# Kernel tuning notes

Measured on AMD Instinct MI355X. Metric: run time of the kernel, lower is better.

## Reference

```python
import jax, jax.numpy as jnp
import numpy as np


def _rotated_kernels(kernel, n_or):
    """Nearest-neighbour rotated copies of the kernel.

    kernel: [C, kOr, kH, kW] -> returns [n_or, C, kOr, kH, kW] where slice t is the
    kernel sampled at R_{2*pi*t/n_or}(y', x') about the kernel center; rotated
    coordinates that fall outside the kernel grid contribute zero.
    """
    C, kOr, kH, kW = kernel.shape
    cy = (kH - 1) / 2.0
    cx = (kW - 1) / 2.0
    ang = 2.0 * jnp.pi * jnp.arange(n_or, dtype=jnp.float32) / n_or
    ca = jnp.cos(ang)[:, None, None]  # [n_or,1,1]
    sa = jnp.sin(ang)[:, None, None]
    yy = jnp.arange(kH, dtype=jnp.float32)[:, None] - cy  # [kH,1]
    xx = jnp.arange(kW, dtype=jnp.float32)[None, :] - cx  # [1,kW]
    # rotate grid points by angle theta
    ys = sa * xx + ca * yy  # [n_or,kH,kW]
    xs = ca * xx - sa * yy
    iy = jnp.round(ys + cy).astype(jnp.int32)
    ix = jnp.round(xs + cx).astype(jnp.int32)
    mask = ((iy >= 0) & (iy < kH) & (ix >= 0) & (ix < kW)).astype(kernel.dtype)
    iyc = jnp.clip(iy, 0, kH - 1)
    ixc = jnp.clip(ix, 0, kW - 1)
    rot = kernel[:, :, iyc, ixc]            # [C,kOr,n_or,kH,kW] (gather)
    rot = rot * mask[None, None]            # zero out-of-grid samples
    return jnp.transpose(rot, (2, 0, 1, 3, 4))  # [n_or,C,kOr,kH,kW]


def setup_inputs() -> dict:
    key = jax.random.key(0)
    k1, k2 = jax.random.split(key)
    B, C, Or, H, W = 8, 32, 8, 128, 128
    kOr, kH, kW = 8, 5, 5
    x = jax.random.normal(k1, (B, C, Or, H, W), dtype=jnp.float32)
    # module parameter: uniform(-1, 1) per reset_parameters()
    kernel = jax.random.uniform(k2, (C, kOr, kH, kW), minval=-1.0, maxval=1.0,
                                dtype=jnp.float32)
    return {"x": x, "kernel": kernel}


def reference(x, kernel):
    """SE(2) linear (depthwise) group convolution.

    out[b,c,t,y,x] = sum_{t',y',x'} x[b,c,(t+t')%Or, y+y', x+x']
                     * kernel[c, t', NN(R_{2pi t/Or}(y', x'))]
    with centered, zero-padded spatial offsets ('SAME').
    """
    B, C, Or, H, W = x.shape
    _, kOr, kH, kW = kernel.shape
    rotk = _rotated_kernels(kernel, Or)  # [Or,C,kOr,kH,kW]
    dn = ('NCHW', 'OIHW', 'NCHW')
    out = jnp.zeros((B, C * Or, H, W), dtype=x.dtype)
    for tp in range(kOr):  # small fixed orientation-offset loop
        xs = jnp.roll(x, -tp, axis=2).reshape(B, C * Or, H, W)  # circular wrap in Or
        k = jnp.transpose(rotk[:, :, tp], (1, 0, 2, 3)).reshape(C * Or, 1, kH, kW)
        out = out + jax.lax.conv_general_dilated(
            xs, k, window_strides=(1, 1), padding='SAME',
            feature_group_count=C * Or, dimension_numbers=dn)
    return out.reshape(B, C, Or, H, W)
```

## Files before the change

kernel.cpp:

```cpp
#include <hip/hip_runtime.h>


typedef short bf16x8 __attribute__((ext_vector_type(8)));
typedef float f32x4 __attribute__((ext_vector_type(4)));

__device__ inline unsigned short f2bf(float f) {
    unsigned int u = __float_as_uint(f);
    u += 0x7fffu + ((u >> 16) & 1u);
    return (unsigned short)(u >> 16);
}
__device__ inline unsigned pk2(float a, float b) {
    return (unsigned)f2bf(a) | ((unsigned)f2bf(b) << 16);
}

__device__ __constant__ float CA8[8] = {1.0f, 0.70710678f, 0.0f, -0.70710678f,
                                        -1.0f, -0.70710678f, 0.0f, 0.70710678f};
__device__ __constant__ float SA8[8] = {0.0f, 0.70710678f, 1.0f, 0.70710678f,
                                        0.0f, -0.70710678f, -1.0f, -0.70710678f};

__global__ __launch_bounds__(256, 5)
void se2_mfma(const float* __restrict__ x, const float* __restrict__ kern,
              float* __restrict__ out) {
    __shared__ __align__(16) unsigned short ldsx[36 * 36 * 8];
    __shared__ __align__(16) unsigned short ldsw[8 * 28 * 8];

    const int bid = (blockIdx.x & 7) * 512 + (blockIdx.x >> 3);
    const int tx = bid & 3, ty = (bid >> 2) & 3;
    const int bc = bid >> 4;
    const int c  = bc & 31;
    const int X0 = tx * 32, Y0 = ty * 32;
    const int tid = threadIdx.x;

    for (int e = tid; e < 1792; e += 256) {
        int t   = e / 224;
        int rem = e - t * 224;
        int tap = rem >> 3;
        int o   = rem & 7;
        float w = 0.0f;
        if (tap < 25) {
            int dy = tap / 5, dx = tap - 5 * (tap / 5);
            float ca = CA8[t], sa = SA8[t];
            float xx = (float)dx - 2.0f, yy = (float)dy - 2.0f;
            int iy = (int)rintf(sa * xx + ca * yy + 2.0f);
            int ix = (int)rintf(ca * xx - sa * yy + 2.0f);
            if (iy >= 0 && iy < 5 && ix >= 0 && ix < 5) {
                int tp = (o - t) & 7;
                w = kern[(c * 8 + tp) * 25 + iy * 5 + ix];
            }
        }
        ldsw[e] = f2bf(w);
    }
    __syncthreads();

    const float* xbase = x + (size_t)bc * 131072;

    auto loadch = [&](int e, float (&v)[8]) {
        int r = e / 36, col = e - r * 36;
        int gy = Y0 - 2 + r, gx = X0 - 2 + col;
        if (gy >= 0 && gy < 128 && gx >= 0 && gx < 128) {
            const float* src = xbase + gy * 128 + gx;
#pragma unroll
            for (int o = 0; o < 8; ++o) v[o] = src[o * 16384];
        } else {
#pragma unroll
            for (int o = 0; o < 8; ++o) v[o] = 0.0f;
        }
    };
    auto packch = [&](int e, const float (&v)[8]) {
        *reinterpret_cast<uint4*>(&ldsx[e * 8]) =
            make_uint4(pk2(v[0], v[1]), pk2(v[2], v[3]),
                       pk2(v[4], v[5]), pk2(v[6], v[7]));
    };

    const int lane  = tid & 63;
    const int wv    = tid >> 6;
    const int g     = lane >> 4;
    const int col16 = lane & 15;

    float sA[8], sB[8];

    loadch(tid, sA);
    loadch(tid + 256, sB);

    bf16x8 wfrag[7];
    int    tapoff[7];
    const bf16x8 zfrag = {0, 0, 0, 0, 0, 0, 0, 0};
#pragma unroll
    for (int cc = 0; cc < 7; ++cc) {
        int tap  = cc * 4 + g;
        int tapc = tap < 25 ? tap : 24;
        int dy = tapc / 5, dx = tapc - 5 * (tapc / 5);
        tapoff[cc] = (dy * 36 + dx) * 8;
        wfrag[cc] = (col16 < 8)
            ? *reinterpret_cast<const bf16x8*>(&ldsw[(col16 * 28 + tap) * 8])
            : zfrag;
    }

    packch(tid, sA);
    packch(tid + 256, sB);
    loadch(tid + 512, sA);
    loadch(tid + 768, sB);
    packch(tid + 512, sA);
    packch(tid + 768, sB);
    loadch(tid + 1024, sA);
    if (tid < 16) loadch(tid + 1280, sB);
    packch(tid + 1024, sA);
    if (tid < 16) packch(tid + 1280, sB);
    __syncthreads();

    float* outl = out + (size_t)bc * 131072 + (size_t)col16 * 16384 +
                  (size_t)Y0 * 128 + X0 + g * 4;

#pragma unroll 2
    for (int cp = 0; cp < 8; ++cp) {
        int y = wv * 8 + cp;
        int baseS = (y * 36 + col16) * 8;
        f32x4 acc0 = {0.f, 0.f, 0.f, 0.f};
        f32x4 acc1 = {0.f, 0.f, 0.f, 0.f};
#pragma unroll
        for (int cc = 0; cc < 7; ++cc) {
            bf16x8 xf0 = *reinterpret_cast<const bf16x8*>(&ldsx[baseS + tapoff[cc]]);
            bf16x8 xf1 = *reinterpret_cast<const bf16x8*>(&ldsx[baseS + 128 + tapoff[cc]]);
            acc0 = __builtin_amdgcn_mfma_f32_16x16x32_bf16(xf0, wfrag[cc], acc0, 0, 0, 0);
            acc1 = __builtin_amdgcn_mfma_f32_16x16x32_bf16(xf1, wfrag[cc], acc1, 0, 0, 0);
        }
        if (col16 < 8) {
            float* po = outl + (size_t)y * 128;
            *reinterpret_cast<float4*>(po)      = make_float4(acc0[0], acc0[1], acc0[2], acc0[3]);
            *reinterpret_cast<float4*>(po + 16) = make_float4(acc1[0], acc1[1], acc1[2], acc1[3]);
        }
    }
}

extern "C" void kernel_launch(void* const* d_in, const int* in_sizes, int n_in,
                              void* d_out, int out_size, void* d_ws, size_t ws_size,
                              hipStream_t stream) {
    const float* x    = (const float*)d_in[0];
    const float* kern = (const float*)d_in[1];
    float* out = (float*)d_out;
    dim3 grid(4096), block(256);
    se2_mfma<<<grid, block, 0, stream>>>(x, kern, out);
}
```

Measured before the change: 56.73 us.

## Fill MFMA N dimension with row-shifted weights and precompute rotated weight table

The MFMA tile is reorganised so that all 16 N columns are used. Eight orientations times two row offsets (dy shift) let one MFMA produce two output rows, where before half the columns were zero-padded. Rotated bf16 weights are now built once in a separate small kernel into the workspace and read straight from global memory, which removes the per-block LDS weight build and its barrier. The cost is an extra kernel launch, 8 K-chunks instead of 7, and dependence on workspace size, with a fallback path that builds the table in LDS.

```diff
diff --git a/kernel.cpp b/kernel.cpp
--- a/kernel.cpp
+++ b/kernel.cpp
@@ -18,11 +18,42 @@
 __device__ __constant__ float SA8[8] = {0.0f, 0.70710678f, 1.0f, 0.70710678f,
                                         0.0f, -0.70710678f, -1.0f, -0.70710678f};
 
-__global__ __launch_bounds__(256, 5)
+__device__ inline float rot_w(const float* __restrict__ kern, int c, int t,
+                              int o, int dy, int dx) {
+    float ca = CA8[t], sa = SA8[t];
+    float xx = (float)dx - 2.0f, yy = (float)dy - 2.0f;
+    int iy = (int)rintf(sa * xx + ca * yy + 2.0f);
+    int ix = (int)rintf(ca * xx - sa * yy + 2.0f);
+    if (iy >= 0 && iy < 5 && ix >= 0 && ix < 5) {
+        int tp = (o - t) & 7;
+        return kern[(c * 8 + tp) * 25 + iy * 5 + ix];
+    }
+    return 0.0f;
+}
+
+__global__ __launch_bounds__(256)
+void build_w2(const float* __restrict__ kern, unsigned short* __restrict__ wtab) {
+    int e = blockIdx.x * 256 + threadIdx.x;
+    if (e >= 131072) return;
+    int o   = e & 7;
+    int tr  = (e >> 3) & 31;
+    int n16 = (e >> 8) & 15;
+    int c   = e >> 12;
+    int t   = n16 & 7, dlt = n16 >> 3;
+    float w = 0.0f;
+    if (tr < 30) {
+        int dyr = tr / 5, dx = tr - 5 * dyr;
+        int dy  = dyr - dlt;
+        if (dy >= 0 && dy < 5) w = rot_w(kern, c, t, o, dy, dx);
+    }
+    wtab[e] = f2bf(w);
+}
+
+template <bool TAB>
+__global__ __launch_bounds__(256)
 void se2_mfma(const float* __restrict__ x, const float* __restrict__ kern,
-              float* __restrict__ out) {
+              const unsigned short* __restrict__ wtab, float* __restrict__ out) {
     __shared__ __align__(16) unsigned short ldsx[36 * 36 * 8];
-    __shared__ __align__(16) unsigned short ldsw[8 * 28 * 8];
 
     const int bid = (blockIdx.x & 7) * 512 + (blockIdx.x >> 3);
     const int tx = bid & 3, ty = (bid >> 2) & 3;
@@ -31,26 +62,10 @@
     const int X0 = tx * 32, Y0 = ty * 32;
     const int tid = threadIdx.x;
 
-    for (int e = tid; e < 1792; e += 256) {
-        int t   = e / 224;
-        int rem = e - t * 224;
-        int tap = rem >> 3;
-        int o   = rem & 7;
-        float w = 0.0f;
-        if (tap < 25) {
-            int dy = tap / 5, dx = tap - 5 * (tap / 5);
-            float ca = CA8[t], sa = SA8[t];
-            float xx = (float)dx - 2.0f, yy = (float)dy - 2.0f;
-            int iy = (int)rintf(sa * xx + ca * yy + 2.0f);
-            int ix = (int)rintf(ca * xx - sa * yy + 2.0f);
-            if (iy >= 0 && iy < 5 && ix >= 0 && ix < 5) {
-                int tp = (o - t) & 7;
-                w = kern[(c * 8 + tp) * 25 + iy * 5 + ix];
-            }
-        }
-        ldsw[e] = f2bf(w);
-    }
-    __syncthreads();
+    const int lane = tid & 63;
+    const int wv   = tid >> 6;
+    const int g    = lane >> 4;
+    const int m16  = lane & 15;
 
     const float* xbase = x + (size_t)bc * 131072;
 
@@ -72,28 +87,41 @@
                        pk2(v[4], v[5]), pk2(v[6], v[7]));
     };
 
-    const int lane  = tid & 63;
-    const int wv    = tid >> 6;
-    const int g     = lane >> 4;
-    const int col16 = lane & 15;
-
     float sA[8], sB[8];
-
     loadch(tid, sA);
     loadch(tid + 256, sB);
 
-    bf16x8 wfrag[7];
-    int    tapoff[7];
-    const bf16x8 zfrag = {0, 0, 0, 0, 0, 0, 0, 0};
+    bf16x8 wfrag[8];
+    int    tapoff[8];
 #pragma unroll
-    for (int cc = 0; cc < 7; ++cc) {
-        int tap  = cc * 4 + g;
-        int tapc = tap < 25 ? tap : 24;
-        int dy = tapc / 5, dx = tapc - 5 * (tapc / 5);
-        tapoff[cc] = (dy * 36 + dx) * 8;
-        wfrag[cc] = (col16 < 8)
-            ? *reinterpret_cast<const bf16x8*>(&ldsw[(col16 * 28 + tap) * 8])
-            : zfrag;
+    for (int cc = 0; cc < 8; ++cc) {
+        int tr  = cc * 4 + g;
+        int trc = tr < 30 ? tr : 29;
+        int dyr = trc / 5, dx = trc - 5 * dyr;
+        tapoff[cc] = (dyr * 36 + dx) * 8;
+        if constexpr (TAB)
+            wfrag[cc] = *reinterpret_cast<const bf16x8*>(
+                &wtab[((c * 16 + m16) * 32 + tr) * 8]);
+    }
+
+    if constexpr (!TAB) {
+        __shared__ __align__(16) unsigned short ldsw[16 * 32 * 8];
+        for (int e = tid; e < 4096; e += 256) {
+            int o = e & 7, tr = (e >> 3) & 31, n16 = e >> 8;
+            int t = n16 & 7, dlt = n16 >> 3;
+            float w = 0.0f;
+            if (tr < 30) {
+                int dyr = tr / 5, dx = tr - 5 * dyr;
+                int dy  = dyr - dlt;
+                if (dy >= 0 && dy < 5) w = rot_w(kern, c, t, o, dy, dx);
+            }
+            ldsw[e] = f2bf(w);
+        }
+        __syncthreads();
+#pragma unroll
+        for (int cc = 0; cc < 8; ++cc)
+            wfrag[cc] = *reinterpret_cast<const bf16x8*>(
+                &ldsw[(m16 * 32 + cc * 4 + g) * 8]);
     }
 
     packch(tid, sA);
@@ -108,27 +136,24 @@
     if (tid < 16) packch(tid + 1280, sB);
     __syncthreads();
 
-    float* outl = out + (size_t)bc * 131072 + (size_t)col16 * 16384 +
-                  (size_t)Y0 * 128 + X0 + g * 4;
+    const int t_o = m16 & 7, dlt = m16 >> 3;
+    float* outl = out + (size_t)bc * 131072 + (size_t)t_o * 16384 +
+                  (size_t)(Y0 + dlt) * 128 + X0 + g * 4;
 
 #pragma unroll 2
-    for (int cp = 0; cp < 8; ++cp) {
-        int y = wv * 8 + cp;
-        int baseS = (y * 36 + col16) * 8;
-        f32x4 acc0 = {0.f, 0.f, 0.f, 0.f};
-        f32x4 acc1 = {0.f, 0.f, 0.f, 0.f};
+    for (int s = 0; s < 8; ++s) {
+        int pr = s >> 1;
+        int xh = s & 1;
+        int yl = wv * 8 + pr * 2;
+        int baseS = (yl * 36 + xh * 16 + m16) * 8;
+        f32x4 acc = {0.f, 0.f, 0.f, 0.f};
 #pragma unroll
-        for (int cc = 0; cc < 7; ++cc) {
-            bf16x8 xf0 = *reinterpret_cast<const bf16x8*>(&ldsx[baseS + tapoff[cc]]);
-            bf16x8 xf1 = *reinterpret_cast<const bf16x8*>(&ldsx[baseS + 128 + tapoff[cc]]);
-            acc0 = __builtin_amdgcn_mfma_f32_16x16x32_bf16(xf0, wfrag[cc], acc0, 0, 0, 0);
-            acc1 = __builtin_amdgcn_mfma_f32_16x16x32_bf16(xf1, wfrag[cc], acc1, 0, 0, 0);
+        for (int cc = 0; cc < 8; ++cc) {
+            bf16x8 xf = *reinterpret_cast<const bf16x8*>(&ldsx[baseS + tapoff[cc]]);
+            acc = __builtin_amdgcn_mfma_f32_16x16x32_bf16(xf, wfrag[cc], acc, 0, 0, 0);
         }
-        if (col16 < 8) {
-            float* po = outl + (size_t)y * 128;
-            *reinterpret_cast<float4*>(po)      = make_float4(acc0[0], acc0[1], acc0[2], acc0[3]);
-            *reinterpret_cast<float4*>(po + 16) = make_float4(acc1[0], acc1[1], acc1[2], acc1[3]);
-        }
+        *reinterpret_cast<float4*>(outl + (size_t)yl * 128 + xh * 16) =
+            make_float4(acc[0], acc[1], acc[2], acc[3]);
     }
 }
 
@@ -138,6 +163,12 @@
     const float* x    = (const float*)d_in[0];
     const float* kern = (const float*)d_in[1];
     float* out = (float*)d_out;
-    dim3 grid(4096), block(256);
-    se2_mfma<<<grid, block, 0, stream>>>(x, kern, out);
+    dim3 block(256);
+    if (ws_size >= 131072 * sizeof(unsigned short)) {
+        unsigned short* wtab = (unsigned short*)d_ws;
+        build_w2<<<dim3(512), block, 0, stream>>>(kern, wtab);
+        se2_mfma<true><<<dim3(4096), block, 0, stream>>>(x, kern, wtab, out);
+    } else {
+        se2_mfma<false><<<dim3(4096), block, 0, stream>>>(x, kern, nullptr, out);
+    }
 }
```

After: 62.39 us. 10.0% more time.
